# Kernel tuning notes

Hardware: AMD Instinct MI355X
Metric: run time of the kernel (lower is better)

The kernel has to match this reference:

```python
import jax, jax.numpy as jnp
import numpy as np

N_NODES = 98304
N_EDGES = 1572864
HIDDEN = 64
N_COMM = 128


def setup_inputs() -> dict:
    key = jax.random.key(0)
    ks = jax.random.split(key, 9)
    return {
        "x_real": jax.random.normal(ks[0], (N_NODES, 1), dtype=jnp.float32),
        "x_imag": jax.random.normal(ks[1], (N_NODES, 1), dtype=jnp.float32),
        "edge_index": jax.random.randint(ks[2], (2, N_EDGES), 0, N_NODES),
        "edge_weight": jax.random.normal(ks[3], (N_EDGES,), dtype=jnp.float32),
        "comm_id": jax.random.randint(ks[4], (N_NODES,), 0, N_COMM),
        "W_local_r": jax.random.normal(ks[5], (HIDDEN, 1), dtype=jnp.float32) * 0.5,
        "W_local_i": jax.random.normal(ks[6], (HIDDEN, 1), dtype=jnp.float32) * 0.5,
        "W_global_r": jax.random.normal(ks[7], (HIDDEN, 1), dtype=jnp.float32) * 0.5,
        "W_global_i": jax.random.normal(ks[8], (HIDDEN, 1), dtype=jnp.float32) * 0.5,
    }


def reference(x_real, x_imag, edge_index, edge_weight, comm_id,
              W_local_r, W_local_i, W_global_r, W_global_i):
    """IntraInterCommunityBlock forward (combine='sum'), complex math as (real, imag) pairs.

    CommunityGNN (1 layer, no bias): complex Linear -> weighted scatter-add
    message passing -> CSiLU (SiLU applied independently to real and imag parts).
    Residual skipped because in_channels=1 != hidden (shape mismatch in source).
    Edge split by community is implemented by zero-masking edge weights, which is
    exactly equivalent for sum aggregation (message = w * x_j).
    """
    n = x_real.shape[0]
    src, dst = edge_index[0], edge_index[1]
    same = comm_id[src] == comm_id[dst]
    ew_intra = jnp.where(same, edge_weight, 0.0)
    ew_inter = jnp.where(same, 0.0, edge_weight)

    def gnn(Wr, Wi, ew):
        # complex linear: (Wr + iWi)(xr + i xi)
        hr = x_real @ Wr.T - x_imag @ Wi.T  # [N, H]
        hi = x_real @ Wi.T + x_imag @ Wr.T  # [N, H]
        # gather -> weight -> scatter-add (aggr='add')
        mr = ew[:, None] * hr[src]  # [E, H]
        mi = ew[:, None] * hi[src]
        ar = jax.ops.segment_sum(mr, dst, num_segments=n)
        ai = jax.ops.segment_sum(mi, dst, num_segments=n)
        # CSiLU: SiLU on real and imag parts
        return jax.nn.silu(ar), jax.nn.silu(ai)

    lr, li = gnn(W_local_r, W_local_i, ew_intra)
    gr, gi = gnn(W_global_r, W_global_i, ew_inter)
    # combine='sum'; stack real/imag on last axis -> [N, H, 2]
    return jnp.stack([lr + gr, li + gi], axis=-1)
```

## Files before the change

kernel.cpp:

```cpp
#include <hip/hip_runtime.h>

#define N_NODES 98304
#define N_EDGES 1572864
#define HIDDEN  64

#define NB      384
#define CAP     4608
#define NBLK    384
#define CHUNK   4096
#define TPB_S   512
#define EPT_S   8
#define SEG     4

#define FP_SCALE 1048576.0f
#define FP_INV   (1.0f / 1048576.0f)

__device__ __forceinline__ float silu_f(float x) {
    return x / (1.0f + __expf(-x));
}


__global__ __launch_bounds__(256) void prep_kernel(const float* __restrict__ xr,
                                                   const float* __restrict__ xi,
                                                   const int* __restrict__ comm,
                                                   float4* __restrict__ node,
                                                   unsigned* __restrict__ ctr)
{
    const int n = blockIdx.x * 256 + threadIdx.x;
    if (blockIdx.x == 0) {
        for (int i = threadIdx.x; i < NB; i += 256) ctr[i] = 0;
    }
    if (n < N_NODES) {
        float4 v;
        v.x = xr[n];
        v.y = xi[n];
        v.z = __int_as_float(comm[n]);
        v.w = 0.0f;
        node[n] = v;
    }
}

__global__ __launch_bounds__(TPB_S) void scatter_kernel(const int* __restrict__ ei,
    const float* __restrict__ ew,
    const float4* __restrict__ node,
    const int* __restrict__ comm,
    unsigned* __restrict__ ctr,
    unsigned long long* __restrict__ payload)
{
    __shared__ unsigned long long sorted[CHUNK];
    __shared__ unsigned short bucketOf[CHUNK];
    __shared__ unsigned hist[NB];
    __shared__ unsigned localbase[NB];
    __shared__ unsigned baseS[NB];

    const int tid = threadIdx.x, blk = blockIdx.x;
    for (int i = tid; i < NB; i += TPB_S) hist[i] = 0;
    __syncthreads();

    const int ebase = blk * CHUNK;
    unsigned long long pay[EPT_S];
    unsigned pb[EPT_S], pr[EPT_S];
#pragma unroll
    for (int k = 0; k < EPT_S; ++k) {
        const int e = ebase + k * TPB_S + tid;
        const int s = ei[e];
        const int d = ei[N_EDGES + e];
        const float w = ew[e];
        const float4 ns = node[s];
        const int cd = comm[d];
        const int dr = __float2int_rn(w * ns.x * FP_SCALE);
        const int di = __float2int_rn(w * ns.y * FP_SCALE);
        const unsigned flag = (__float_as_int(ns.z) == cd) ? 0u : 1u;
        const unsigned b = (unsigned)d >> 8;
        pb[k] = b;
        pr[k] = atomicAdd(&hist[b], 1u);
        pay[k] = ((unsigned long long)((unsigned)dr & 0x07FFFFFFu) << 37)
               | ((unsigned long long)((unsigned)di & 0x07FFFFFFu) << 10)
               | ((unsigned)(d & 255) << 2) | ((unsigned long long)flag << 1);
    }
    __syncthreads();

    if (tid < 64) {
        unsigned v[6];
        unsigned s = 0;
#pragma unroll
        for (int m = 0; m < 6; ++m) { v[m] = hist[tid * 6 + m]; s += v[m]; }
        unsigned p = s;
#pragma unroll
        for (int off = 1; off < 64; off <<= 1) {
            unsigned t = __shfl_up(p, off);
            if (tid >= off) p += t;
        }
        unsigned excl = p - s;
#pragma unroll
        for (int m = 0; m < 6; ++m) { unsigned t = v[m]; localbase[tid * 6 + m] = excl; excl += t; }
    }
    __syncthreads();

    for (int i = tid; i < NB; i += TPB_S)
        baseS[i] = (unsigned)i * CAP + atomicAdd(&ctr[i], hist[i]);
#pragma unroll
    for (int k = 0; k < EPT_S; ++k) {
        const unsigned pos = localbase[pb[k]] + pr[k];
        sorted[pos] = pay[k];
        bucketOf[pos] = (unsigned short)pb[k];
    }
    __syncthreads();

    for (int i = tid; i < CHUNK; i += TPB_S) {
        const unsigned b = bucketOf[i];
        const unsigned slot = baseS[b] + ((unsigned)i - localbase[b]);
        if (slot < ((unsigned)b + 1u) * CAP)
            payload[slot] = sorted[i];
    }
}

__global__ __launch_bounds__(256) void accum_partial_kernel(
    const unsigned long long* __restrict__ payload,
    const unsigned* __restrict__ ctr,
    int* __restrict__ partial)
{
    __shared__ int accR[512];
    __shared__ int accI[512];
    const int tid = threadIdx.x;
    const int bucket = blockIdx.x >> 2;
    const int seg = blockIdx.x & 3;
    accR[tid] = 0; accR[tid + 256] = 0;
    accI[tid] = 0; accI[tid + 256] = 0;
    __syncthreads();

    unsigned cnt = ctr[bucket];
    if (cnt > CAP) cnt = CAP;
    const unsigned start = (cnt * (unsigned)seg) >> 2;
    const unsigned end   = (cnt * (unsigned)(seg + 1)) >> 2;
    const unsigned long long* buck = payload + (size_t)bucket * CAP;
    for (unsigned i = start + tid; i < end; i += 256) {
        const unsigned long long p = buck[i];
        const int dr = (int)((long long)p >> 37);
        const int di = (int)(((long long)(p << 27)) >> 37);
        const unsigned idx = (((unsigned)(p >> 2) & 255u) << 1) | ((unsigned)(p >> 1) & 1u);
        atomicAdd(&accR[idx], dr);
        atomicAdd(&accI[idx], di);
    }
    __syncthreads();

    int* base = partial + ((size_t)blockIdx.x << 10);
    base[tid]       = accR[tid];
    base[tid + 256] = accR[tid + 256];
    base[tid + 512] = accI[tid];
    base[tid + 768] = accI[tid + 256];
}

__global__ __launch_bounds__(256) void final_epilogue_kernel(
    const int* __restrict__ partial,
    const float* __restrict__ Wlr, const float* __restrict__ Wli,
    const float* __restrict__ Wgr, const float* __restrict__ Wgi,
    float4* __restrict__ out)
{
    __shared__ float sR[32][2];
    __shared__ float sI[32][2];
    __shared__ float2 w_s[4][32];
    const int tid = threadIdx.x, blk = blockIdx.x;
    const int bucket = blk >> 3;
    const int obase  = (blk & 7) * 32;

    if (tid < 64) {
        const int ln  = tid >> 1;
        const int sel = tid & 1;
        const int aidx = obase * 2 + tid;
        int sumR = 0, sumI = 0;
#pragma unroll
        for (int seg = 0; seg < SEG; ++seg) {
            const int* reg = partial + ((size_t)(bucket * SEG + seg) << 10);
            sumR += reg[aidx];
            sumI += reg[512 + aidx];
        }
        sR[ln][sel] = (float)sumR * FP_INV;
        sI[ln][sel] = (float)sumI * FP_INV;
    } else if (tid >= 128) {
        const int t = tid - 128;
        const int which = t >> 5, h2 = t & 31;
        const float* W = (which == 0) ? Wlr : (which == 1) ? Wli
                       : (which == 2) ? Wgr : Wgi;
        w_s[which][h2] = ((const float2*)W)[h2];
    }
    __syncthreads();

#pragma unroll
    for (int j = 0; j < 4; ++j) {
        const int idx = j * 256 + tid;
        const int ln  = idx >> 5;
        const int h2  = idx & 31;
        const float sr_l = sR[ln][0], si_l = sI[ln][0];
        const float sr_g = sR[ln][1], si_g = sI[ln][1];
        const float2 a = w_s[0][h2], c = w_s[1][h2];
        const float2 g = w_s[2][h2], f = w_s[3][h2];
        float4 o;
        {
            const float arl = a.x * sr_l - c.x * si_l;
            const float ail = c.x * sr_l + a.x * si_l;
            const float arg = g.x * sr_g - f.x * si_g;
            const float aig = f.x * sr_g + g.x * si_g;
            o.x = silu_f(arl) + silu_f(arg);
            o.y = silu_f(ail) + silu_f(aig);
        }
        {
            const float arl = a.y * sr_l - c.y * si_l;
            const float ail = c.y * sr_l + a.y * si_l;
            const float arg = g.y * sr_g - f.y * si_g;
            const float aig = f.y * sr_g + g.y * si_g;
            o.z = silu_f(arl) + silu_f(arg);
            o.w = silu_f(ail) + silu_f(aig);
        }
        out[(size_t)blk * 1024 + idx] = o;
    }
}


#define FB_SCALE 2097152.0f
#define FB_INV   (1.0f / 2097152.0f)

__global__ void edge_scatter_fb(const int* __restrict__ ei,
                                const float* __restrict__ ew,
                                const int* __restrict__ comm,
                                const float* __restrict__ xr,
                                const float* __restrict__ xi,
                                unsigned long long* __restrict__ P)
{
    const int e = blockIdx.x * blockDim.x + threadIdx.x;
    if (e >= N_EDGES) return;
    const int s = ei[e];
    const int d = ei[N_EDGES + e];
    const float w = ew[e];
    const int dr = __float2int_rn(w * xr[s] * FB_SCALE);
    const int di = __float2int_rn(w * xi[s] * FB_SCALE);
    const unsigned long long delta =
        (unsigned long long)(((long long)dr << 32) + (long long)di);
    const int base = (comm[s] == comm[d]) ? 0 : N_NODES;
    atomicAdd(&P[base + d], delta);
}

__global__ void epilogue_fb(const unsigned long long* __restrict__ P,
                            const float* __restrict__ Wlr,
                            const float* __restrict__ Wli,
                            const float* __restrict__ Wgr,
                            const float* __restrict__ Wgi,
                            float4* __restrict__ out)
{
    const int total = N_NODES * (HIDDEN / 2);
    const int t = blockIdx.x * blockDim.x + threadIdx.x;
    if (t >= total) return;
    const int n = t >> 5, h2 = t & 31;
    float sr_l, si_l, sr_g, si_g;
    {
        const unsigned long long U = P[n];
        const int bi = (int)(unsigned)(U & 0xffffffffULL);
        const int ar = (int)(unsigned)(U >> 32) + (bi < 0 ? 1 : 0);
        sr_l = (float)ar * FB_INV; si_l = (float)bi * FB_INV;
    }
    {
        const unsigned long long U = P[N_NODES + n];
        const int bi = (int)(unsigned)(U & 0xffffffffULL);
        const int ar = (int)(unsigned)(U >> 32) + (bi < 0 ? 1 : 0);
        sr_g = (float)ar * FB_INV; si_g = (float)bi * FB_INV;
    }
    const float2 wlr = ((const float2*)Wlr)[h2];
    const float2 wli = ((const float2*)Wli)[h2];
    const float2 wgr = ((const float2*)Wgr)[h2];
    const float2 wgi = ((const float2*)Wgi)[h2];
    float4 o;
    {
        const float arl = wlr.x * sr_l - wli.x * si_l;
        const float ail = wli.x * sr_l + wlr.x * si_l;
        const float arg = wgr.x * sr_g - wgi.x * si_g;
        const float aig = wgi.x * sr_g + wgr.x * si_g;
        o.x = silu_f(arl) + silu_f(arg);
        o.y = silu_f(ail) + silu_f(aig);
    }
    {
        const float arl = wlr.y * sr_l - wli.y * si_l;
        const float ail = wli.y * sr_l + wlr.y * si_l;
        const float arg = wgr.y * sr_g - wgi.y * si_g;
        const float aig = wgi.y * sr_g + wgr.y * si_g;
        o.z = silu_f(arl) + silu_f(arg);
        o.w = silu_f(ail) + silu_f(aig);
    }
    out[t] = o;
}

extern "C" void kernel_launch(void* const* d_in, const int* in_sizes, int n_in,
                              void* d_out, int out_size, void* d_ws, size_t ws_size,
                              hipStream_t stream) {
    const float* xr   = (const float*)d_in[0];
    const float* xi   = (const float*)d_in[1];
    const int*   ei   = (const int*)d_in[2];
    const float* ew   = (const float*)d_in[3];
    const int*   comm = (const int*)d_in[4];
    const float* Wlr  = (const float*)d_in[5];
    const float* Wli  = (const float*)d_in[6];
    const float* Wgr  = (const float*)d_in[7];
    const float* Wgi  = (const float*)d_in[8];

    const size_t payload_bytes = (size_t)NB * CAP * sizeof(unsigned long long);
    const size_t ctr_bytes     = 4096;
    const size_t node_bytes    = (size_t)N_NODES * sizeof(float4);
    const size_t partial_bytes = (size_t)NB * SEG * 1024 * sizeof(int);
    const size_t need = payload_bytes + ctr_bytes + node_bytes + partial_bytes;

    if (ws_size >= need) {
        char* p = (char*)d_ws;
        unsigned long long* payload = (unsigned long long*)p;  p += payload_bytes;
        unsigned* ctr               = (unsigned*)p;            p += ctr_bytes;
        float4* node                = (float4*)p;              p += node_bytes;
        int* partial                = (int*)p;

        hipLaunchKernelGGL(prep_kernel, dim3(N_NODES / 256), dim3(256), 0, stream,
                           xr, xi, comm, node, ctr);
        hipLaunchKernelGGL(scatter_kernel, dim3(NBLK), dim3(TPB_S), 0, stream,
                           ei, ew, node, comm, ctr, payload);
        hipLaunchKernelGGL(accum_partial_kernel, dim3(NB * SEG), dim3(256), 0, stream,
                           payload, ctr, partial);
        hipLaunchKernelGGL(final_epilogue_kernel, dim3(N_NODES / 32), dim3(256), 0, stream,
                           partial, Wlr, Wli, Wgr, Wgi, (float4*)d_out);
    } else {
        unsigned long long* P = (unsigned long long*)d_ws;
        hipMemsetAsync(P, 0, (size_t)2 * N_NODES * sizeof(unsigned long long), stream);
        hipLaunchKernelGGL(edge_scatter_fb, dim3((N_EDGES + 255) / 256), dim3(256), 0, stream,
                           ei, ew, comm, xr, xi, P);
        const int total = N_NODES * (HIDDEN / 2);
        hipLaunchKernelGGL(epilogue_fb, dim3((total + 255) / 256), dim3(256), 0, stream,
                           P, Wlr, Wli, Wgr, Wgi, (float4*)d_out);
    }
}
```

Before: 57.57 us.

## Fuse bucket accumulation with epilogue and drop node-packing prep kernel

Removes the prep kernel that packed x and community ids into float4 nodes, so the scatter kernel gathers xr, xi and comm directly and a memset zeroes the counters. The per-bucket partial accumulation and final epilogue become one kernel. Each block scans its whole bucket and keeps only the 64-node quarter it owns, accumulating in shared memory and writing SiLU outputs directly. This cuts two launches and the partial-sum round trip through global memory, at the cost of each block reading its full bucket (4x redundant payload reads) and extra scattered gathers in scatter_kernel.

Measured after the change: 70.47 us. +22.4%, slower.

```diff
diff --git a/kernel.cpp b/kernel.cpp
--- a/kernel.cpp
+++ b/kernel.cpp
@@ -20,29 +20,10 @@
 }
 
 
-__global__ __launch_bounds__(256) void prep_kernel(const float* __restrict__ xr,
-                                                   const float* __restrict__ xi,
-                                                   const int* __restrict__ comm,
-                                                   float4* __restrict__ node,
-                                                   unsigned* __restrict__ ctr)
-{
-    const int n = blockIdx.x * 256 + threadIdx.x;
-    if (blockIdx.x == 0) {
-        for (int i = threadIdx.x; i < NB; i += 256) ctr[i] = 0;
-    }
-    if (n < N_NODES) {
-        float4 v;
-        v.x = xr[n];
-        v.y = xi[n];
-        v.z = __int_as_float(comm[n]);
-        v.w = 0.0f;
-        node[n] = v;
-    }
-}
-
 __global__ __launch_bounds__(TPB_S) void scatter_kernel(const int* __restrict__ ei,
     const float* __restrict__ ew,
-    const float4* __restrict__ node,
+    const float* __restrict__ xr,
+    const float* __restrict__ xi,
     const int* __restrict__ comm,
     unsigned* __restrict__ ctr,
     unsigned long long* __restrict__ payload)
@@ -66,11 +47,11 @@
         const int s = ei[e];
         const int d = ei[N_EDGES + e];
         const float w = ew[e];
-        const float4 ns = node[s];
-        const int cd = comm[d];
-        const int dr = __float2int_rn(w * ns.x * FP_SCALE);
-        const int di = __float2int_rn(w * ns.y * FP_SCALE);
-        const unsigned flag = (__float_as_int(ns.z) == cd) ? 0u : 1u;
+        const float vr = xr[s];
+        const float vi = xi[s];
+        const int dr = __float2int_rn(w * vr * FP_SCALE);
+        const int di = __float2int_rn(w * vi * FP_SCALE);
+        const unsigned flag = (comm[s] == comm[d]) ? 0u : 1u;
         const unsigned b = (unsigned)d >> 8;
         pb[k] = b;
         pr[k] = atomicAdd(&hist[b], 1u);
@@ -115,69 +96,24 @@
     }
 }
 
-__global__ __launch_bounds__(256) void accum_partial_kernel(
+__global__ __launch_bounds__(256) void accum_epilogue_kernel(
     const unsigned long long* __restrict__ payload,
     const unsigned* __restrict__ ctr,
-    int* __restrict__ partial)
-{
-    __shared__ int accR[512];
-    __shared__ int accI[512];
-    const int tid = threadIdx.x;
-    const int bucket = blockIdx.x >> 2;
-    const int seg = blockIdx.x & 3;
-    accR[tid] = 0; accR[tid + 256] = 0;
-    accI[tid] = 0; accI[tid + 256] = 0;
-    __syncthreads();
-
-    unsigned cnt = ctr[bucket];
-    if (cnt > CAP) cnt = CAP;
-    const unsigned start = (cnt * (unsigned)seg) >> 2;
-    const unsigned end   = (cnt * (unsigned)(seg + 1)) >> 2;
-    const unsigned long long* buck = payload + (size_t)bucket * CAP;
-    for (unsigned i = start + tid; i < end; i += 256) {
-        const unsigned long long p = buck[i];
-        const int dr = (int)((long long)p >> 37);
-        const int di = (int)(((long long)(p << 27)) >> 37);
-        const unsigned idx = (((unsigned)(p >> 2) & 255u) << 1) | ((unsigned)(p >> 1) & 1u);
-        atomicAdd(&accR[idx], dr);
-        atomicAdd(&accI[idx], di);
-    }
-    __syncthreads();
-
-    int* base = partial + ((size_t)blockIdx.x << 10);
-    base[tid]       = accR[tid];
-    base[tid + 256] = accR[tid + 256];
-    base[tid + 512] = accI[tid];
-    base[tid + 768] = accI[tid + 256];
-}
-
-__global__ __launch_bounds__(256) void final_epilogue_kernel(
-    const int* __restrict__ partial,
     const float* __restrict__ Wlr, const float* __restrict__ Wli,
     const float* __restrict__ Wgr, const float* __restrict__ Wgi,
     float4* __restrict__ out)
 {
-    __shared__ float sR[32][2];
-    __shared__ float sI[32][2];
+    __shared__ int accR[128];
+    __shared__ int accI[128];
     __shared__ float2 w_s[4][32];
-    const int tid = threadIdx.x, blk = blockIdx.x;
-    const int bucket = blk >> 3;
-    const int obase  = (blk & 7) * 32;
-
-    if (tid < 64) {
-        const int ln  = tid >> 1;
-        const int sel = tid & 1;
-        const int aidx = obase * 2 + tid;
-        int sumR = 0, sumI = 0;
-#pragma unroll
-        for (int seg = 0; seg < SEG; ++seg) {
-            const int* reg = partial + ((size_t)(bucket * SEG + seg) << 10);
-            sumR += reg[aidx];
-            sumI += reg[512 + aidx];
-        }
-        sR[ln][sel] = (float)sumR * FP_INV;
-        sI[ln][sel] = (float)sumI * FP_INV;
-    } else if (tid >= 128) {
+    const int tid = threadIdx.x;
+    const int x    = blockIdx.x & 7;
+    const int slot = blockIdx.x >> 3;
+    const int bucket = x * (NB / 8) + (slot >> 2);
+    const int seg    = slot & 3;
+
+    if (tid < 128) { accR[tid] = 0; accI[tid] = 0; }
+    else {
         const int t = tid - 128;
         const int which = t >> 5, h2 = t & 31;
         const float* W = (which == 0) ? Wlr : (which == 1) ? Wli
@@ -186,13 +122,31 @@
     }
     __syncthreads();
 
-#pragma unroll
-    for (int j = 0; j < 4; ++j) {
+    unsigned cnt = ctr[bucket];
+    if (cnt > CAP) cnt = CAP;
+    const unsigned long long* buck = payload + (size_t)bucket * CAP;
+    for (unsigned i = tid; i < cnt; i += 256) {
+        const unsigned long long p = buck[i];
+        const unsigned ln = (unsigned)(p >> 2) & 255u;
+        if ((int)(ln >> 6) == seg) {
+            const int dr = (int)((long long)p >> 37);
+            const int di = (int)(((long long)(p << 27)) >> 37);
+            const unsigned idx = ((ln & 63u) << 1) | ((unsigned)(p >> 1) & 1u);
+            atomicAdd(&accR[idx], dr);
+            atomicAdd(&accI[idx], di);
+        }
+    }
+    __syncthreads();
+
+#pragma unroll
+    for (int j = 0; j < 8; ++j) {
         const int idx = j * 256 + tid;
         const int ln  = idx >> 5;
         const int h2  = idx & 31;
-        const float sr_l = sR[ln][0], si_l = sI[ln][0];
-        const float sr_g = sR[ln][1], si_g = sI[ln][1];
+        const float sr_l = (float)accR[ln * 2 + 0] * FP_INV;
+        const float si_l = (float)accI[ln * 2 + 0] * FP_INV;
+        const float sr_g = (float)accR[ln * 2 + 1] * FP_INV;
+        const float si_g = (float)accI[ln * 2 + 1] * FP_INV;
         const float2 a = w_s[0][h2], c = w_s[1][h2];
         const float2 g = w_s[2][h2], f = w_s[3][h2];
         float4 o;
@@ -212,7 +166,7 @@
             o.z = silu_f(arl) + silu_f(arg);
             o.w = silu_f(ail) + silu_f(aig);
         }
-        out[(size_t)blk * 1024 + idx] = o;
+        out[(size_t)bucket * 8192 + (size_t)seg * 2048 + idx] = o;
     }
 }
 
@@ -303,25 +257,18 @@
 
     const size_t payload_bytes = (size_t)NB * CAP * sizeof(unsigned long long);
     const size_t ctr_bytes     = 4096;
-    const size_t node_bytes    = (size_t)N_NODES * sizeof(float4);
-    const size_t partial_bytes = (size_t)NB * SEG * 1024 * sizeof(int);
-    const size_t need = payload_bytes + ctr_bytes + node_bytes + partial_bytes;
+    const size_t need = payload_bytes + ctr_bytes;
 
     if (ws_size >= need) {
         char* p = (char*)d_ws;
         unsigned long long* payload = (unsigned long long*)p;  p += payload_bytes;
-        unsigned* ctr               = (unsigned*)p;            p += ctr_bytes;
-        float4* node                = (float4*)p;              p += node_bytes;
-        int* partial                = (int*)p;
-
-        hipLaunchKernelGGL(prep_kernel, dim3(N_NODES / 256), dim3(256), 0, stream,
-                           xr, xi, comm, node, ctr);
+        unsigned* ctr               = (unsigned*)p;
+
+        hipMemsetAsync(ctr, 0, NB * sizeof(unsigned), stream);
         hipLaunchKernelGGL(scatter_kernel, dim3(NBLK), dim3(TPB_S), 0, stream,
-                           ei, ew, node, comm, ctr, payload);
-        hipLaunchKernelGGL(accum_partial_kernel, dim3(NB * SEG), dim3(256), 0, stream,
-                           payload, ctr, partial);
-        hipLaunchKernelGGL(final_epilogue_kernel, dim3(N_NODES / 32), dim3(256), 0, stream,
-                           partial, Wlr, Wli, Wgr, Wgi, (float4*)d_out);
+                           ei, ew, xr, xi, comm, ctr, payload);
+        hipLaunchKernelGGL(accum_epilogue_kernel, dim3(NB * SEG), dim3(256), 0, stream,
+                           payload, ctr, Wlr, Wli, Wgr, Wgi, (float4*)d_out);
     } else {
         unsigned long long* P = (unsigned long long*)d_ws;
         hipMemsetAsync(P, 0, (size_t)2 * N_NODES * sizeof(unsigned long long), stream);
```

## Replace global bucket counters with per-chunk local offsets and contiguous payload writes

Applied to the files above, without the earlier changes.

The scatter kernel no longer reserves slots in global per-bucket regions with atomics. Each block now writes its locally sorted chunk contiguously and stores its per-bucket local base offsets in a table. The accumulate kernel walks that offset table to find each bucket's slice in every chunk. This removes the global atomics, the counter reset, the CAP overflow truncation and the scattered uncoalesced writes. In exchange the accumulate kernel does irregular per-thread serial loops over short, unevenly sized slices. Chunks also shrink to 1024 edges so the offsets fit in 16 bits.

After: 58.51 us. About the same (+1.6%).

```diff
diff --git a/kernel.cpp b/kernel.cpp
--- a/kernel.cpp
+++ b/kernel.cpp
@@ -5,12 +5,12 @@
 #define HIDDEN  64
 
 #define NB      384
-#define CAP     4608
-#define NBLK    384
-#define CHUNK   4096
-#define TPB_S   512
-#define EPT_S   8
+#define NBLK    1536
+#define CHUNK   1024
+#define TPB_S   256
+#define EPT_S   4
 #define SEG     4
+#define CPS     (NBLK / SEG)
 
 #define FP_SCALE 1048576.0f
 #define FP_INV   (1.0f / 1048576.0f)
@@ -23,13 +23,9 @@
 __global__ __launch_bounds__(256) void prep_kernel(const float* __restrict__ xr,
                                                    const float* __restrict__ xi,
                                                    const int* __restrict__ comm,
-                                                   float4* __restrict__ node,
-                                                   unsigned* __restrict__ ctr)
+                                                   float4* __restrict__ node)
 {
     const int n = blockIdx.x * 256 + threadIdx.x;
-    if (blockIdx.x == 0) {
-        for (int i = threadIdx.x; i < NB; i += 256) ctr[i] = 0;
-    }
     if (n < N_NODES) {
         float4 v;
         v.x = xr[n];
@@ -44,14 +40,12 @@
     const float* __restrict__ ew,
     const float4* __restrict__ node,
     const int* __restrict__ comm,
-    unsigned* __restrict__ ctr,
+    unsigned short* __restrict__ lbT,
     unsigned long long* __restrict__ payload)
 {
     __shared__ unsigned long long sorted[CHUNK];
-    __shared__ unsigned short bucketOf[CHUNK];
     __shared__ unsigned hist[NB];
     __shared__ unsigned localbase[NB];
-    __shared__ unsigned baseS[NB];
 
     const int tid = threadIdx.x, blk = blockIdx.x;
     for (int i = tid; i < NB; i += TPB_S) hist[i] = 0;
@@ -97,27 +91,20 @@
     }
     __syncthreads();
 
+#pragma unroll
+    for (int k = 0; k < EPT_S; ++k)
+        sorted[localbase[pb[k]] + pr[k]] = pay[k];
     for (int i = tid; i < NB; i += TPB_S)
-        baseS[i] = (unsigned)i * CAP + atomicAdd(&ctr[i], hist[i]);
-#pragma unroll
-    for (int k = 0; k < EPT_S; ++k) {
-        const unsigned pos = localbase[pb[k]] + pr[k];
-        sorted[pos] = pay[k];
-        bucketOf[pos] = (unsigned short)pb[k];
-    }
-    __syncthreads();
-
-    for (int i = tid; i < CHUNK; i += TPB_S) {
-        const unsigned b = bucketOf[i];
-        const unsigned slot = baseS[b] + ((unsigned)i - localbase[b]);
-        if (slot < ((unsigned)b + 1u) * CAP)
-            payload[slot] = sorted[i];
-    }
+        lbT[(size_t)blk * NB + i] = (unsigned short)localbase[i];
+    __syncthreads();
+
+    for (int i = tid; i < CHUNK; i += TPB_S)
+        payload[(size_t)blk * CHUNK + i] = sorted[i];
 }
 
 __global__ __launch_bounds__(256) void accum_partial_kernel(
     const unsigned long long* __restrict__ payload,
-    const unsigned* __restrict__ ctr,
+    const unsigned short* __restrict__ lbT,
     int* __restrict__ partial)
 {
     __shared__ int accR[512];
@@ -129,18 +116,22 @@
     accI[tid] = 0; accI[tid + 256] = 0;
     __syncthreads();
 
-    unsigned cnt = ctr[bucket];
-    if (cnt > CAP) cnt = CAP;
-    const unsigned start = (cnt * (unsigned)seg) >> 2;
-    const unsigned end   = (cnt * (unsigned)(seg + 1)) >> 2;
-    const unsigned long long* buck = payload + (size_t)bucket * CAP;
-    for (unsigned i = start + tid; i < end; i += 256) {
-        const unsigned long long p = buck[i];
-        const int dr = (int)((long long)p >> 37);
-        const int di = (int)(((long long)(p << 27)) >> 37);
-        const unsigned idx = (((unsigned)(p >> 2) & 255u) << 1) | ((unsigned)(p >> 1) & 1u);
-        atomicAdd(&accR[idx], dr);
-        atomicAdd(&accI[idx], di);
+    const int c0 = seg * CPS;
+    for (int cc = tid; cc < CPS; cc += 256) {
+        const int c = c0 + cc;
+        const unsigned base = lbT[(size_t)c * NB + bucket];
+        const unsigned next = (bucket < NB - 1)
+                            ? (unsigned)lbT[(size_t)c * NB + bucket + 1]
+                            : (unsigned)CHUNK;
+        const unsigned long long* chunkp = payload + (size_t)c * CHUNK;
+        for (unsigned i = base; i < next; ++i) {
+            const unsigned long long p = chunkp[i];
+            const int dr = (int)((long long)p >> 37);
+            const int di = (int)(((long long)(p << 27)) >> 37);
+            const unsigned idx = (((unsigned)(p >> 2) & 255u) << 1) | ((unsigned)(p >> 1) & 1u);
+            atomicAdd(&accR[idx], dr);
+            atomicAdd(&accI[idx], di);
+        }
     }
     __syncthreads();
 
@@ -301,25 +292,25 @@
     const float* Wgr  = (const float*)d_in[7];
     const float* Wgi  = (const float*)d_in[8];
 
-    const size_t payload_bytes = (size_t)NB * CAP * sizeof(unsigned long long);
-    const size_t ctr_bytes     = 4096;
+    const size_t payload_bytes = (size_t)N_EDGES * sizeof(unsigned long long);
+    const size_t lbT_bytes     = (size_t)NBLK * NB * sizeof(unsigned short);
     const size_t node_bytes    = (size_t)N_NODES * sizeof(float4);
     const size_t partial_bytes = (size_t)NB * SEG * 1024 * sizeof(int);
-    const size_t need = payload_bytes + ctr_bytes + node_bytes + partial_bytes;
+    const size_t need = payload_bytes + lbT_bytes + node_bytes + partial_bytes;
 
     if (ws_size >= need) {
         char* p = (char*)d_ws;
         unsigned long long* payload = (unsigned long long*)p;  p += payload_bytes;
-        unsigned* ctr               = (unsigned*)p;            p += ctr_bytes;
+        unsigned short* lbT         = (unsigned short*)p;      p += lbT_bytes;
         float4* node                = (float4*)p;              p += node_bytes;
         int* partial                = (int*)p;
 
         hipLaunchKernelGGL(prep_kernel, dim3(N_NODES / 256), dim3(256), 0, stream,
-                           xr, xi, comm, node, ctr);
+                           xr, xi, comm, node);
         hipLaunchKernelGGL(scatter_kernel, dim3(NBLK), dim3(TPB_S), 0, stream,
-                           ei, ew, node, comm, ctr, payload);
+                           ei, ew, node, comm, lbT, payload);
         hipLaunchKernelGGL(accum_partial_kernel, dim3(NB * SEG), dim3(256), 0, stream,
-                           payload, ctr, partial);
+                           payload, lbT, partial);
         hipLaunchKernelGGL(final_epilogue_kernel, dim3(N_NODES / 32), dim3(256), 0, stream,
                            partial, Wlr, Wli, Wgr, Wgi, (float4*)d_out);
     } else {
```
